# Kernel tuning notes

Hardware: AMD Instinct MI355X
Metric: run time of the kernel (lower is better)

Reference implementation:

```python
import jax, jax.numpy as jnp
import numpy as np

N = 20000      # nodes
E = 320000     # edges (before self-loops)
IN = 128       # in_channels
D = 256        # hidden_channels (d_model)
H = 8          # nhead
DH = D // H    # d_head
L = 2          # num_layers
B = 64         # NUM_DEGREE_BUCKETS
DFF = 2 * D    # dim_ff = d*2 per source


def setup_inputs() -> dict:
    key = jax.random.key(0)
    ks = jax.random.split(key, 24)
    w = lambda k, s: (jax.random.normal(k, s, jnp.float32) * 0.02)
    x = jax.random.normal(ks[0], (N, IN), jnp.float32)
    row = jax.random.randint(ks[1], (E,), 0, N, jnp.int32)
    col = jax.random.randint(ks[2], (E,), 0, N, jnp.int32)
    deg_emb = w(ks[3], (B, D)).at[0].set(0.0)  # padding_idx=0
    return dict(
        x=x, row=row, col=col,
        Wx=w(ks[4], (IN, D)), bx=jnp.zeros((D,), jnp.float32),
        deg_emb=deg_emb,
        sb=w(ks[5], (L, B, H)),
        Wq=w(ks[6], (L, D, D)), bq=jnp.zeros((L, D), jnp.float32),
        Wk=w(ks[7], (L, D, D)), bk=jnp.zeros((L, D), jnp.float32),
        Wv=w(ks[8], (L, D, D)), bv=jnp.zeros((L, D), jnp.float32),
        Wo=w(ks[9], (L, D, D)), bo=jnp.zeros((L, D), jnp.float32),
        ln1_g=jnp.ones((L, D), jnp.float32), ln1_b=jnp.zeros((L, D), jnp.float32),
        ln2_g=jnp.ones((L, D), jnp.float32), ln2_b=jnp.zeros((L, D), jnp.float32),
        W1=w(ks[10], (L, D, DFF)), b1=jnp.zeros((L, DFF), jnp.float32),
        W2=w(ks[11], (L, DFF, D)), b2=jnp.zeros((L, D), jnp.float32),
    )


def _ln(x, g, b):
    m = x.mean(-1, keepdims=True)
    v = ((x - m) ** 2).mean(-1, keepdims=True)
    return (x - m) / jnp.sqrt(v + 1e-5) * g + b


def reference(x, row, col, Wx, bx, deg_emb, sb, Wq, bq, Wk, bk, Wv, bv, Wo, bo,
              ln1_g, ln1_b, ln2_g, ln2_b, W1, b1, W2, b2):
    n = x.shape[0]
    # degree from original adjacency (before self loops)
    deg = jax.ops.segment_sum(jnp.ones_like(row, jnp.float32), row, num_segments=n)
    bucket = jnp.clip(jnp.floor(jnp.log2(jnp.maximum(deg, 1.0))), 1, B - 1).astype(jnp.int32)
    h = x @ Wx + bx + deg_emb[bucket]
    # set_diag(): append self loops
    sl = jnp.arange(n, dtype=row.dtype)
    r = jnp.concatenate([row, sl])
    c = jnp.concatenate([col, sl])
    scale = DH ** -0.5
    for i in range(L):
        Q = (h @ Wq[i] + bq[i]).reshape(n, H, DH)
        K = (h @ Wk[i] + bk[i]).reshape(n, H, DH)
        V = (h @ Wv[i] + bv[i]).reshape(n, H, DH)
        # per-edge multi-head scores + degree-bucket spatial bias  [E_tot, H]
        scores = (Q[r] * K[c]).sum(-1) * scale + sb[i][bucket[r]] + sb[i][bucket[c]]
        mx = jax.ops.segment_max(scores, r, num_segments=n)
        es = jnp.exp(scores - mx[r])
        ss = jax.ops.segment_sum(es, r, num_segments=n)
        alpha = es / jnp.maximum(ss[r], 1e-12)
        agg = jax.ops.segment_sum(alpha[:, :, None] * V[c], r, num_segments=n).reshape(n, D)
        out = agg @ Wo[i] + bo[i]
        h = _ln(h + out, ln1_g[i], ln1_b[i])
        ff = jax.nn.gelu(h @ W1[i] + b1[i], approximate=False) @ W2[i] + b2[i]
        h = _ln(h + ff, ln2_g[i], ln2_b[i])
    return h
```

## Files before the change

kernel.cpp:

```cpp
#include <hip/hip_runtime.h>
#include <hip/hip_bf16.h>
#include <math.h>

#define NNODES 20000
#define NEDGES 320000
#define INC 128
#define DMODEL 256
#define NHEAD 8
#define DHEAD 32
#define NLAYER 2
#define NBUCKET 64
#define DFF 512
#define ETOT (NEDGES + NNODES)
#define UNR 8

typedef __attribute__((ext_vector_type(8))) short short8v;
typedef __attribute__((ext_vector_type(4))) float f32x4;

__device__ __forceinline__ float bf2f(unsigned short u) {
    return __uint_as_float(((unsigned int)u) << 16);
}
__device__ __forceinline__ unsigned short f2bf(float f) {
    unsigned int u = __float_as_uint(f);
    unsigned int r = (u + 0x7FFFu + ((u >> 16) & 1u)) >> 16;
    return (unsigned short)r;
}

__global__ void count_deg_k(const int* __restrict__ row, int* __restrict__ deg, int E) {
    int e = blockIdx.x * 256 + threadIdx.x;
    if (e < E) atomicAdd(&deg[row[e]], 1);
}

__global__ void bucket_k(const int* __restrict__ deg, int* __restrict__ bkt, int n) {
    int i = blockIdx.x * 256 + threadIdx.x;
    if (i < n) {
        int d = deg[i]; if (d < 1) d = 1;
        int b = 31 - __clz(d);
        b = min(max(b, 1), NBUCKET - 1);
        bkt[i] = b;
    }
}

__global__ __launch_bounds__(1024) void scan_offsets_k(const int* __restrict__ deg,
                                                       int* __restrict__ off,
                                                       int* __restrict__ cur, int n) {
    const int T = 1024;
    int t = threadIdx.x;
    int chunk = (n + T - 1) / T;
    int base = t * chunk;
    int s = 0;
    for (int i = 0; i < chunk; ++i) {
        int idx = base + i;
        if (idx < n) s += deg[idx] + 1;
    }
    __shared__ int ps[1024];
    ps[t] = s;
    __syncthreads();
    for (int d = 1; d < T; d <<= 1) {
        int v = (t >= d) ? ps[t - d] : 0;
        __syncthreads();
        ps[t] += v;
        __syncthreads();
    }
    int run = (t == 0) ? 0 : ps[t - 1];
    for (int i = 0; i < chunk; ++i) {
        int idx = base + i;
        if (idx < n) {
            off[idx] = run; cur[idx] = run;
            run += deg[idx] + 1;
        }
    }
    if (t == T - 1) off[n] = ps[T - 1];
}

__global__ void csr_fill_k(const int* __restrict__ row, const int* __restrict__ col,
                           const int* __restrict__ bkt,
                           int* __restrict__ cur, int* __restrict__ csr, int E, int n) {
    int e = blockIdx.x * 256 + threadIdx.x;
    if (e < E) {
        int c = col[e];
        int p = atomicAdd(&cur[row[e]], 1);
        csr[p] = c | (bkt[c] << 19);
    } else if (e < E + n) {
        int nn = e - E;
        int p = atomicAdd(&cur[nn], 1);
        csr[p] = nn | (bkt[nn] << 19);
    }
}

__global__ void cvt_bf16_k(const float* __restrict__ s, unsigned short* __restrict__ d, int n) {
    int i = (blockIdx.x * 256 + threadIdx.x) * 4;
    if (i < n) {
        float4 v = *(const float4*)(s + i);
        ushort4 o;
        o.x = f2bf(v.x); o.y = f2bf(v.y); o.z = f2bf(v.z); o.w = f2bf(v.w);
        *(ushort4*)(d + i) = o;
    }
}

__global__ __launch_bounds__(256) void transpose_cvt_k(const float* __restrict__ src,
                                                       unsigned short* __restrict__ dst,
                                                       int K, int N) {
    __shared__ float tile[32][33];
    const int k0 = blockIdx.y * 32;
    const int n0 = blockIdx.x * 32;
    const int t = threadIdx.x;
    {
        int r = t >> 3, c = (t & 7) * 4;
        float4 v = *(const float4*)(src + (size_t)(k0 + r) * N + n0 + c);
        tile[r][c] = v.x; tile[r][c + 1] = v.y; tile[r][c + 2] = v.z; tile[r][c + 3] = v.w;
    }
    __syncthreads();
    {
        int n = t >> 3, k = (t & 7) * 4;
        ushort4 o;
        o.x = f2bf(tile[k][n]); o.y = f2bf(tile[k + 1][n]);
        o.z = f2bf(tile[k + 2][n]); o.w = f2bf(tile[k + 3][n]);
        *(ushort4*)(dst + (size_t)(n0 + n) * K + k0 + k) = o;
    }
}

__global__ void concat3_k(const float* a, const float* b, const float* c, float* d) {
    int t = blockIdx.x * 256 + threadIdx.x;
    if (t < 256) d[t] = a[t];
    else if (t < 512) d[t] = b[t - 256];
    else if (t < 768) d[t] = c[t - 512];
}

__global__ __launch_bounds__(256) void gemm_bf16_k(
        const unsigned short* __restrict__ A, const unsigned short* __restrict__ Wt,
        const float* __restrict__ bias,
        float* __restrict__ Cf, unsigned short* __restrict__ Cb,
        int M, int K, int Nout,
        const float* __restrict__ emb, const int* __restrict__ bkt, int act) {
    __shared__ unsigned short As[128 * 40];
    __shared__ unsigned short Bs[128 * 40];
    const int bm = blockIdx.x * 128;
    const int bn = blockIdx.y * 128;
    const int t = threadIdx.x;
    const int wid = t >> 6, lane = t & 63;
    const int wm = wid >> 1, wn = wid & 1;
    const int l16 = lane & 15, kslc = lane >> 4;

    f32x4 acc[4][4] = {};

    const int mrow = t >> 1, half = t & 1;
    for (int k0 = 0; k0 < K; k0 += 32) {
        {
            const unsigned short* srcA = A + (size_t)(bm + mrow) * K + k0 + half * 16;
            uint4 v0 = {0, 0, 0, 0}, v1 = {0, 0, 0, 0};
            if (bm + mrow < M) {
                v0 = *(const uint4*)srcA;
                v1 = *(const uint4*)(srcA + 8);
            }
            *(uint4*)(&As[mrow * 40 + half * 16]) = v0;
            *(uint4*)(&As[mrow * 40 + half * 16 + 8]) = v1;
            const unsigned short* srcB = Wt + (size_t)(bn + mrow) * K + k0 + half * 16;
            *(uint4*)(&Bs[mrow * 40 + half * 16]) = *(const uint4*)srcB;
            *(uint4*)(&Bs[mrow * 40 + half * 16 + 8]) = *(const uint4*)(srcB + 8);
        }
        __syncthreads();
        short8v a[4], b[4];
        #pragma unroll
        for (int f = 0; f < 4; ++f) {
            a[f] = *(const short8v*)(&As[(wm * 64 + f * 16 + l16) * 40 + kslc * 8]);
            b[f] = *(const short8v*)(&Bs[(wn * 64 + f * 16 + l16) * 40 + kslc * 8]);
        }
        #pragma unroll
        for (int fm = 0; fm < 4; ++fm)
            #pragma unroll
            for (int fn = 0; fn < 4; ++fn)
                acc[fm][fn] = __builtin_amdgcn_mfma_f32_16x16x32_bf16(
                    a[fm], b[fn], acc[fm][fn], 0, 0, 0);
        __syncthreads();
    }

    #pragma unroll
    for (int fm = 0; fm < 4; ++fm) {
        #pragma unroll
        for (int fn = 0; fn < 4; ++fn) {
            int cc = wn * 64 + fn * 16 + l16;
            int gn = bn + cc;
            float bn_v = bias[gn];
            int rbase = bm + wm * 64 + fm * 16 + (lane >> 4) * 4;
            #pragma unroll
            for (int r = 0; r < 4; ++r) {
                int gm = rbase + r;
                if (gm >= M) continue;
                float v = acc[fm][fn][r] + bn_v;
                if (emb) v += emb[(size_t)bkt[gm] * Nout + gn];
                if (act) v = 0.5f * v * (1.f + erff(v * 0.70710678118654752f));
                if (Cf) Cf[(size_t)gm * Nout + gn] = v;
                if (Cb) Cb[(size_t)gm * Nout + gn] = f2bf(v);
            }
        }
    }
}


#define LOADB(CC, KK, VV, SB, J)                                               \
    do {                                                                        \
        _Pragma("unroll")                                                       \
        for (int e = 0; e < UNR; ++e)                                           \
            CC[e] = csr[min((J) + e, s1 - 1)];                                  \
        _Pragma("unroll")                                                       \
        for (int e = 0; e < UNR; ++e) {                                         \
            const unsigned short* base =                                        \
                QKV + (size_t)(CC[e] & 0x7FFFF) * 768 + hh * 32 + d2 * 2;       \
            KK[e] = *(const ushort2*)(base + 256);                              \
            VV[e] = *(const ushort2*)(base + 512);                              \
            SB[e] = sb_i[(CC[e] >> 19) * NHEAD + hh];                           \
        }                                                                       \
    } while (0)

#define COMPUTE(KK, VV, SB, J)                                                 \
    do {                                                                        \
        _Pragma("unroll")                                                       \
        for (int e = 0; e < UNR; ++e) {                                         \
            float p = qx * bf2f(KK[e].x) + qy * bf2f(KK[e].y);                  \
            _Pragma("unroll")                                                   \
            for (int mk = 8; mk >= 1; mk >>= 1) p += __shfl_xor(p, mk);         \
            float sc = p * scale + sbn + SB[e];                                 \
            if ((J) + e < s1) {                                                 \
                float mn = fmaxf(m, sc);                                        \
                float corr = __expf(m - mn);                                    \
                float es = __expf(sc - mn);                                     \
                s = s * corr + es;                                              \
                ax = ax * corr + es * bf2f(VV[e].x);                            \
                ay = ay * corr + es * bf2f(VV[e].y);                            \
                m = mn;                                                         \
            }                                                                   \
        }                                                                       \
    } while (0)

__global__ __launch_bounds__(128) void attn_bf16_k(
        const unsigned short* __restrict__ QKV,
        const int* __restrict__ off, const int* __restrict__ csr,
        const int* __restrict__ bkt, const float* __restrict__ sb_i,
        unsigned short* __restrict__ aggb) {
    const int node = blockIdx.x;
    const int t = threadIdx.x;
    const int hh = t >> 4, d2 = t & 15;
    const int s0 = off[node], s1 = off[node + 1];
    const ushort2 q2 = *(const ushort2*)(QKV + (size_t)node * 768 + hh * 32 + d2 * 2);
    const float qx = bf2f(q2.x), qy = bf2f(q2.y);
    const float sbn = sb_i[bkt[node] * NHEAD + hh];
    const float scale = 0.17677669529663689f;
    float m = -1e30f, s = 0.f, ax = 0.f, ay = 0.f;

    int ccA[UNR]; ushort2 kkA[UNR], vvA[UNR]; float sbA[UNR];
    int ccB[UNR]; ushort2 kkB[UNR], vvB[UNR]; float sbB[UNR];

    LOADB(ccA, kkA, vvA, sbA, s0);
    for (int j = s0; j < s1; j += 2 * UNR) {
        LOADB(ccB, kkB, vvB, sbB, j + UNR);
        COMPUTE(kkA, vvA, sbA, j);
        LOADB(ccA, kkA, vvA, sbA, j + 2 * UNR);
        COMPUTE(kkB, vvB, sbB, j + UNR);
    }

    float inv = 1.f / fmaxf(s, 1e-12f);
    ushort2 o;
    o.x = f2bf(ax * inv); o.y = f2bf(ay * inv);
    *(ushort2*)(aggb + (size_t)node * DMODEL + hh * 32 + d2 * 2) = o;
}

__global__ __launch_bounds__(256) void add_ln_k(float* __restrict__ h,
                                                const float* __restrict__ add,
                                                const float* __restrict__ g,
                                                const float* __restrict__ b,
                                                unsigned short* __restrict__ hb) {
    const int r = blockIdx.x;
    const int t = threadIdx.x;
    float x = h[(size_t)r * DMODEL + t] + add[(size_t)r * DMODEL + t];
    __shared__ float red[4];
    float s = x;
    #pragma unroll
    for (int mk = 32; mk >= 1; mk >>= 1) s += __shfl_xor(s, mk);
    if ((t & 63) == 0) red[t >> 6] = s;
    __syncthreads();
    float mean = (red[0] + red[1] + red[2] + red[3]) * (1.f / DMODEL);
    float dx = x - mean;
    __syncthreads();
    float v = dx * dx;
    #pragma unroll
    for (int mk = 32; mk >= 1; mk >>= 1) v += __shfl_xor(v, mk);
    if ((t & 63) == 0) red[t >> 6] = v;
    __syncthreads();
    float var = (red[0] + red[1] + red[2] + red[3]) * (1.f / DMODEL);
    float y = dx * rsqrtf(var + 1e-5f) * g[t] + b[t];
    h[(size_t)r * DMODEL + t] = y;
    hb[(size_t)r * DMODEL + t] = f2bf(y);
}

extern "C" void kernel_launch(void* const* d_in, const int* in_sizes, int n_in,
                              void* d_out, int out_size, void* d_ws, size_t ws_size,
                              hipStream_t stream) {
    const float* x      = (const float*)d_in[0];
    const int*   row    = (const int*)d_in[1];
    const int*   col    = (const int*)d_in[2];
    const float* Wx     = (const float*)d_in[3];
    const float* bx     = (const float*)d_in[4];
    const float* degemb = (const float*)d_in[5];
    const float* sb     = (const float*)d_in[6];
    const float* Wq     = (const float*)d_in[7];
    const float* bq     = (const float*)d_in[8];
    const float* Wk     = (const float*)d_in[9];
    const float* bk     = (const float*)d_in[10];
    const float* Wv     = (const float*)d_in[11];
    const float* bv     = (const float*)d_in[12];
    const float* Wo     = (const float*)d_in[13];
    const float* bo     = (const float*)d_in[14];
    const float* ln1g   = (const float*)d_in[15];
    const float* ln1b   = (const float*)d_in[16];
    const float* ln2g   = (const float*)d_in[17];
    const float* ln2b   = (const float*)d_in[18];
    const float* W1     = (const float*)d_in[19];
    const float* b1     = (const float*)d_in[20];
    const float* W2     = (const float*)d_in[21];
    const float* b2     = (const float*)d_in[22];

    const int Nn = NNODES, E = NEDGES;
    float* h = (float*)d_out;

    char* w = (char*)d_ws;
    unsigned short* hb   = (unsigned short*)w; w += (size_t)Nn * DMODEL * 2;
    unsigned short* QKVb = (unsigned short*)w; w += (size_t)Nn * 768 * 2;
    unsigned short* AGGb = (unsigned short*)w; w += (size_t)Nn * DMODEL * 2;
    unsigned short* FFb  = (unsigned short*)w; w += (size_t)Nn * DFF * 2;
    float*          OUT  = (float*)w;          w += (size_t)Nn * DMODEL * 4;
    unsigned short* xb   = (unsigned short*)w; w += (size_t)Nn * INC * 2;
    unsigned short* Wxt  = (unsigned short*)w; w += (size_t)DMODEL * INC * 2;
    unsigned short* Wqkvt[NLAYER]; float* bqkv[NLAYER];
    unsigned short *Wot[NLAYER], *W1t[NLAYER], *W2t[NLAYER];
    for (int l = 0; l < NLAYER; ++l) {
        Wqkvt[l] = (unsigned short*)w; w += (size_t)768 * DMODEL * 2;
        bqkv[l]  = (float*)w;          w += 768 * 4;
        Wot[l]   = (unsigned short*)w; w += (size_t)DMODEL * DMODEL * 2;
        W1t[l]   = (unsigned short*)w; w += (size_t)DFF * DMODEL * 2;
        W2t[l]   = (unsigned short*)w; w += (size_t)DMODEL * DFF * 2;
    }
    int* CSR = (int*)w; w += (size_t)ETOT * 4;
    int* OFF = (int*)w; w += (Nn + 1) * 4;
    int* CUR = (int*)w; w += Nn * 4;
    int* DEG = (int*)w; w += Nn * 4;
    int* BKT = (int*)w; w += Nn * 4;

    hipMemsetAsync(DEG, 0, Nn * sizeof(int), stream);
    count_deg_k<<<(E + 255) / 256, 256, 0, stream>>>(row, DEG, E);
    bucket_k<<<(Nn + 255) / 256, 256, 0, stream>>>(DEG, BKT, Nn);
    scan_offsets_k<<<1, 1024, 0, stream>>>(DEG, OFF, CUR, Nn);
    csr_fill_k<<<(E + Nn + 255) / 256, 256, 0, stream>>>(row, col, BKT, CUR, CSR, E, Nn);

    cvt_bf16_k<<<((size_t)Nn * INC / 4 + 255) / 256, 256, 0, stream>>>(x, xb, Nn * INC);
    {
        dim3 g(DMODEL / 32, INC / 32);
        transpose_cvt_k<<<g, 256, 0, stream>>>(Wx, Wxt, INC, DMODEL);
    }
    for (int l = 0; l < NLAYER; ++l) {
        const size_t DD = (size_t)DMODEL * DMODEL;
        dim3 gDD(DMODEL / 32, DMODEL / 32);
        transpose_cvt_k<<<gDD, 256, 0, stream>>>(Wq + l * DD, Wqkvt[l],                DMODEL, DMODEL);
        transpose_cvt_k<<<gDD, 256, 0, stream>>>(Wk + l * DD, Wqkvt[l] + 256 * DMODEL, DMODEL, DMODEL);
        transpose_cvt_k<<<gDD, 256, 0, stream>>>(Wv + l * DD, Wqkvt[l] + 512 * DMODEL, DMODEL, DMODEL);
        concat3_k<<<3, 256, 0, stream>>>(bq + l * DMODEL, bk + l * DMODEL, bv + l * DMODEL, bqkv[l]);
        transpose_cvt_k<<<gDD, 256, 0, stream>>>(Wo + l * DD, Wot[l], DMODEL, DMODEL);
        dim3 g1(DFF / 32, DMODEL / 32);
        transpose_cvt_k<<<g1, 256, 0, stream>>>(W1 + (size_t)l * DMODEL * DFF, W1t[l], DMODEL, DFF);
        dim3 g2(DMODEL / 32, DFF / 32);
        transpose_cvt_k<<<g2, 256, 0, stream>>>(W2 + (size_t)l * DFF * DMODEL, W2t[l], DFF, DMODEL);
    }

    const int MB = (Nn + 127) / 128;

    {
        dim3 grid(MB, DMODEL / 128);
        gemm_bf16_k<<<grid, 256, 0, stream>>>(xb, Wxt, bx, h, hb, Nn, INC, DMODEL,
                                              degemb, BKT, 0);
    }

    for (int l = 0; l < NLAYER; ++l) {
        const float* sb_i = sb + (size_t)l * NBUCKET * NHEAD;
        dim3 gQKV(MB, 768 / 128);
        dim3 gD(MB, DMODEL / 128);
        dim3 gF(MB, DFF / 128);

        gemm_bf16_k<<<gQKV, 256, 0, stream>>>(hb, Wqkvt[l], bqkv[l], nullptr, QKVb,
                                              Nn, DMODEL, 768, nullptr, nullptr, 0);
        attn_bf16_k<<<Nn, 128, 0, stream>>>(QKVb, OFF, CSR, BKT, sb_i, AGGb);
        gemm_bf16_k<<<gD, 256, 0, stream>>>(AGGb, Wot[l], bo + (size_t)l * DMODEL,
                                            OUT, nullptr, Nn, DMODEL, DMODEL,
                                            nullptr, nullptr, 0);
        add_ln_k<<<Nn, 256, 0, stream>>>(h, OUT, ln1g + (size_t)l * DMODEL,
                                         ln1b + (size_t)l * DMODEL, hb);
        gemm_bf16_k<<<gF, 256, 0, stream>>>(hb, W1t[l], b1 + (size_t)l * DFF,
                                            nullptr, FFb, Nn, DMODEL, DFF,
                                            nullptr, nullptr, 1);
        gemm_bf16_k<<<gD, 256, 0, stream>>>(FFb, W2t[l], b2 + (size_t)l * DMODEL,
                                            OUT, nullptr, Nn, DFF, DMODEL,
                                            nullptr, nullptr, 0);
        add_ln_k<<<Nn, 256, 0, stream>>>(h, OUT, ln2g + (size_t)l * DMODEL,
                                         ln2b + (size_t)l * DMODEL, hb);
    }
}
```

Baseline: 649.7 us.

## Batch weight transposes into one launch and use direct global-to-LDS loads in GEMM

Merges the bucket computation into the scan kernel, folds thirteen weight transpose launches and two bias concatenations into single launches, and rewrites the GEMM tile loads to use global_load_lds (direct global-to-LDS DMA) with an unpadded LDS layout. Activation buffers are padded to a multiple of 128 rows so the loads can drop the bounds check. The aim is fewer kernel launches and cheaper staging of GEMM operands. The trade-off is possible LDS bank conflicts from removing the padding, and padded rows now being read uninitialised, which only feed output rows that are never stored.

```diff
diff --git a/kernel.cpp b/kernel.cpp
--- a/kernel.cpp
+++ b/kernel.cpp
@@ -3,6 +3,7 @@
 #include <math.h>
 
 #define NNODES 20000
+#define NPAD   20096
 #define NEDGES 320000
 #define INC 128
 #define DMODEL 256
@@ -25,25 +26,21 @@
     unsigned int r = (u + 0x7FFFu + ((u >> 16) & 1u)) >> 16;
     return (unsigned short)r;
 }
+__device__ __forceinline__ void gl16(const unsigned short* g, unsigned short* l) {
+    __builtin_amdgcn_global_load_lds(
+        (const __attribute__((address_space(1))) void*)g,
+        (__attribute__((address_space(3))) void*)l, 16, 0, 0);
+}
 
 __global__ void count_deg_k(const int* __restrict__ row, int* __restrict__ deg, int E) {
     int e = blockIdx.x * 256 + threadIdx.x;
     if (e < E) atomicAdd(&deg[row[e]], 1);
 }
 
-__global__ void bucket_k(const int* __restrict__ deg, int* __restrict__ bkt, int n) {
-    int i = blockIdx.x * 256 + threadIdx.x;
-    if (i < n) {
-        int d = deg[i]; if (d < 1) d = 1;
-        int b = 31 - __clz(d);
-        b = min(max(b, 1), NBUCKET - 1);
-        bkt[i] = b;
-    }
-}
-
 __global__ __launch_bounds__(1024) void scan_offsets_k(const int* __restrict__ deg,
                                                        int* __restrict__ off,
-                                                       int* __restrict__ cur, int n) {
+                                                       int* __restrict__ cur,
+                                                       int* __restrict__ bkt, int n) {
     const int T = 1024;
     int t = threadIdx.x;
     int chunk = (n + T - 1) / T;
@@ -51,7 +48,13 @@
     int s = 0;
     for (int i = 0; i < chunk; ++i) {
         int idx = base + i;
-        if (idx < n) s += deg[idx] + 1;
+        if (idx < n) {
+            int d = deg[idx];
+            int dd = d < 1 ? 1 : d;
+            int b = 31 - __clz(dd);
+            bkt[idx] = min(max(b, 1), NBUCKET - 1);
+            s += d + 1;
+        }
     }
     __shared__ int ps[1024];
     ps[t] = s;
@@ -98,12 +101,22 @@
     }
 }
 
-__global__ __launch_bounds__(256) void transpose_cvt_k(const float* __restrict__ src,
-                                                       unsigned short* __restrict__ dst,
-                                                       int K, int N) {
+struct TDesc { const float* src; unsigned short* dst; int K; int N; int tileStart; };
+struct TPack { TDesc d[13]; int nd; };
+
+__global__ __launch_bounds__(256) void mega_transpose_k(TPack p) {
     __shared__ float tile[32][33];
-    const int k0 = blockIdx.y * 32;
-    const int n0 = blockIdx.x * 32;
+    const int tb = blockIdx.x;
+    int di = 0;
+    for (int i = 1; i < 13; ++i)
+        if (i < p.nd && p.d[i].tileStart <= tb) di = i;
+    const float* __restrict__ src = p.d[di].src;
+    unsigned short* __restrict__ dst = p.d[di].dst;
+    const int K = p.d[di].K, N = p.d[di].N;
+    const int local = tb - p.d[di].tileStart;
+    const int tpn = N >> 5;
+    const int n0 = (local % tpn) * 32;
+    const int k0 = (local / tpn) * 32;
     const int t = threadIdx.x;
     {
         int r = t >> 3, c = (t & 7) * 4;
@@ -120,11 +133,16 @@
     }
 }
 
-__global__ void concat3_k(const float* a, const float* b, const float* c, float* d) {
+__global__ void concat_bias2_k(const float* __restrict__ bq, const float* __restrict__ bk,
+                               const float* __restrict__ bv,
+                               float* __restrict__ d0, float* __restrict__ d1) {
     int t = blockIdx.x * 256 + threadIdx.x;
-    if (t < 256) d[t] = a[t];
-    else if (t < 512) d[t] = b[t - 256];
-    else if (t < 768) d[t] = c[t - 512];
+    int l = t / 768, u = t - l * 768;
+    float v;
+    if (u < 256) v = bq[l * DMODEL + u];
+    else if (u < 512) v = bk[l * DMODEL + u - 256];
+    else v = bv[l * DMODEL + u - 512];
+    (l ? d1 : d0)[u] = v;
 }
 
 __global__ __launch_bounds__(256) void gemm_bf16_k(
@@ -133,38 +151,31 @@
         float* __restrict__ Cf, unsigned short* __restrict__ Cb,
         int M, int K, int Nout,
         const float* __restrict__ emb, const int* __restrict__ bkt, int act) {
-    __shared__ unsigned short As[128 * 40];
-    __shared__ unsigned short Bs[128 * 40];
+    __shared__ unsigned short As[128 * 32];
+    __shared__ unsigned short Bs[128 * 32];
     const int bm = blockIdx.x * 128;
     const int bn = blockIdx.y * 128;
     const int t = threadIdx.x;
     const int wid = t >> 6, lane = t & 63;
     const int wm = wid >> 1, wn = wid & 1;
     const int l16 = lane & 15, kslc = lane >> 4;
+    const int srow = lane >> 2, scol = (lane & 3) * 8;
 
     f32x4 acc[4][4] = {};
 
-    const int mrow = t >> 1, half = t & 1;
     for (int k0 = 0; k0 < K; k0 += 32) {
-        {
-            const unsigned short* srcA = A + (size_t)(bm + mrow) * K + k0 + half * 16;
-            uint4 v0 = {0, 0, 0, 0}, v1 = {0, 0, 0, 0};
-            if (bm + mrow < M) {
-                v0 = *(const uint4*)srcA;
-                v1 = *(const uint4*)(srcA + 8);
-            }
-            *(uint4*)(&As[mrow * 40 + half * 16]) = v0;
-            *(uint4*)(&As[mrow * 40 + half * 16 + 8]) = v1;
-            const unsigned short* srcB = Wt + (size_t)(bn + mrow) * K + k0 + half * 16;
-            *(uint4*)(&Bs[mrow * 40 + half * 16]) = *(const uint4*)srcB;
-            *(uint4*)(&Bs[mrow * 40 + half * 16 + 8]) = *(const uint4*)(srcB + 8);
-        }
+        const unsigned short* gA = A + (size_t)(bm + wid * 32 + srow) * K + k0 + scol;
+        const unsigned short* gB = Wt + (size_t)(bn + wid * 32 + srow) * K + k0 + scol;
+        gl16(gA,          &As[(wid * 32) * 32]);
+        gl16(gA + 16 * K, &As[(wid * 32 + 16) * 32]);
+        gl16(gB,          &Bs[(wid * 32) * 32]);
+        gl16(gB + 16 * K, &Bs[(wid * 32 + 16) * 32]);
         __syncthreads();
         short8v a[4], b[4];
         #pragma unroll
         for (int f = 0; f < 4; ++f) {
-            a[f] = *(const short8v*)(&As[(wm * 64 + f * 16 + l16) * 40 + kslc * 8]);
-            b[f] = *(const short8v*)(&Bs[(wn * 64 + f * 16 + l16) * 40 + kslc * 8]);
+            a[f] = *(const short8v*)(&As[(wm * 64 + f * 16 + l16) * 32 + kslc * 8]);
+            b[f] = *(const short8v*)(&Bs[(wn * 64 + f * 16 + l16) * 32 + kslc * 8]);
         }
         #pragma unroll
         for (int fm = 0; fm < 4; ++fm)
@@ -324,12 +335,12 @@
     float* h = (float*)d_out;
 
     char* w = (char*)d_ws;
-    unsigned short* hb   = (unsigned short*)w; w += (size_t)Nn * DMODEL * 2;
+    unsigned short* hb   = (unsigned short*)w; w += (size_t)NPAD * DMODEL * 2;
     unsigned short* QKVb = (unsigned short*)w; w += (size_t)Nn * 768 * 2;
-    unsigned short* AGGb = (unsigned short*)w; w += (size_t)Nn * DMODEL * 2;
-    unsigned short* FFb  = (unsigned short*)w; w += (size_t)Nn * DFF * 2;
+    unsigned short* AGGb = (unsigned short*)w; w += (size_t)NPAD * DMODEL * 2;
+    unsigned short* FFb  = (unsigned short*)w; w += (size_t)NPAD * DFF * 2;
     float*          OUT  = (float*)w;          w += (size_t)Nn * DMODEL * 4;
-    unsigned short* xb   = (unsigned short*)w; w += (size_t)Nn * INC * 2;
+    unsigned short* xb   = (unsigned short*)w; w += (size_t)NPAD * INC * 2;
     unsigned short* Wxt  = (unsigned short*)w; w += (size_t)DMODEL * INC * 2;
     unsigned short* Wqkvt[NLAYER]; float* bqkv[NLAYER];
     unsigned short *Wot[NLAYER], *W1t[NLAYER], *W2t[NLAYER];
@@ -348,27 +359,31 @@
 
     hipMemsetAsync(DEG, 0, Nn * sizeof(int), stream);
     count_deg_k<<<(E + 255) / 256, 256, 0, stream>>>(row, DEG, E);
-    bucket_k<<<(Nn + 255) / 256, 256, 0, stream>>>(DEG, BKT, Nn);
-    scan_offsets_k<<<1, 1024, 0, stream>>>(DEG, OFF, CUR, Nn);
+    scan_offsets_k<<<1, 1024, 0, stream>>>(DEG, OFF, CUR, BKT, Nn);
     csr_fill_k<<<(E + Nn + 255) / 256, 256, 0, stream>>>(row, col, BKT, CUR, CSR, E, Nn);
 
     cvt_bf16_k<<<((size_t)Nn * INC / 4 + 255) / 256, 256, 0, stream>>>(x, xb, Nn * INC);
     {
-        dim3 g(DMODEL / 32, INC / 32);
-        transpose_cvt_k<<<g, 256, 0, stream>>>(Wx, Wxt, INC, DMODEL);
-    }
-    for (int l = 0; l < NLAYER; ++l) {
+        TPack pk; int nd = 0, tt = 0;
+        auto add = [&](const float* s, unsigned short* d, int K, int N) {
+            pk.d[nd].src = s; pk.d[nd].dst = d; pk.d[nd].K = K; pk.d[nd].N = N;
+            pk.d[nd].tileStart = tt;
+            tt += (K / 32) * (N / 32);
+            ++nd;
+        };
         const size_t DD = (size_t)DMODEL * DMODEL;
-        dim3 gDD(DMODEL / 32, DMODEL / 32);
-        transpose_cvt_k<<<gDD, 256, 0, stream>>>(Wq + l * DD, Wqkvt[l],                DMODEL, DMODEL);
-        transpose_cvt_k<<<gDD, 256, 0, stream>>>(Wk + l * DD, Wqkvt[l] + 256 * DMODEL, DMODEL, DMODEL);
-        transpose_cvt_k<<<gDD, 256, 0, stream>>>(Wv + l * DD, Wqkvt[l] + 512 * DMODEL, DMODEL, DMODEL);
-        concat3_k<<<3, 256, 0, stream>>>(bq + l * DMODEL, bk + l * DMODEL, bv + l * DMODEL, bqkv[l]);
-        transpose_cvt_k<<<gDD, 256, 0, stream>>>(Wo + l * DD, Wot[l], DMODEL, DMODEL);
-        dim3 g1(DFF / 32, DMODEL / 32);
-        transpose_cvt_k<<<g1, 256, 0, stream>>>(W1 + (size_t)l * DMODEL * DFF, W1t[l], DMODEL, DFF);
-        dim3 g2(DMODEL / 32, DFF / 32);
-        transpose_cvt_k<<<g2, 256, 0, stream>>>(W2 + (size_t)l * DFF * DMODEL, W2t[l], DFF, DMODEL);
+        add(Wx, Wxt, INC, DMODEL);
+        for (int l = 0; l < NLAYER; ++l) {
+            add(Wq + l * DD, Wqkvt[l],                DMODEL, DMODEL);
+            add(Wk + l * DD, Wqkvt[l] + 256 * DMODEL, DMODEL, DMODEL);
+            add(Wv + l * DD, Wqkvt[l] + 512 * DMODEL, DMODEL, DMODEL);
+            add(Wo + l * DD, Wot[l], DMODEL, DMODEL);
+            add(W1 + (size_t)l * DMODEL * DFF, W1t[l], DMODEL, DFF);
+            add(W2 + (size_t)l * DFF * DMODEL, W2t[l], DFF, DMODEL);
+        }
+        pk.nd = nd;
+        mega_transpose_k<<<tt, 256, 0, stream>>>(pk);
+        concat_bias2_k<<<6, 256, 0, stream>>>(bq, bk, bv, bqkv[0], bqkv[1]);
     }
 
     const int MB = (Nn + 127) / 128;
```

New measurement: 638.1 us. No clear change (-1.8%).
